# Optimization experiments

Measured on AMD Instinct MI355X. Metric: run time of the kernel, lower is better.

The kernel has to match this reference:

```python
import jax, jax.numpy as jnp
import numpy as np

EPS = 1e-9

def _gumbel_softmax(logits, u):
    # torch: noise.add_(1e-9).log_().neg_() twice -> g = -log(-log(u+eps)+eps)
    g = -jnp.log(-jnp.log(u + EPS) + EPS)
    return jax.nn.softmax(logits + g, axis=-1)  # tau=1, temperature=0

def setup_inputs() -> dict:
    key = jax.random.key(0)
    ks = jax.random.split(key, 8)
    n_obs, n_topics, n_dim, batch = 8192, 128, 64, 8192
    return {
        "pij": jax.random.uniform(ks[0], (batch,), jnp.float32, 1e-6, 1.0),
        "noise_full": jax.random.uniform(ks[1], (n_obs, n_topics), jnp.float32),
        "noise_i": jax.random.uniform(ks[2], (batch, n_topics), jnp.float32),
        "noise_j": jax.random.uniform(ks[3], (batch, n_topics), jnp.float32),
        "logits_weight": jax.random.normal(ks[4], (n_obs, n_topics), jnp.float32),
        "topic_w": jax.random.normal(ks[5], (n_dim, n_topics), jnp.float32) * 0.1,
        "topic_b": jax.random.normal(ks[6], (n_dim,), jnp.float32) * 0.1,
        "i": jax.random.randint(ks[7], (batch,), 0, n_obs),
        "j": jax.random.randint(jax.random.fold_in(key, 7), (batch,), 0, n_obs),
    }

def reference(pij, noise_full, noise_i, noise_j, logits_weight, topic_w, topic_b, i, j):
    topic = lambda z: z @ topic_w.T + topic_b
    # x: [n_obs, n_dim]
    x = topic(_gumbel_softmax(logits_weight, noise_full))
    # pairwise squared distances via norm trick (same math as expand-sub-square-sum)
    sq = jnp.sum(x * x, axis=-1)                      # [n_obs]
    dkl2 = sq[:, None] + sq[None, :] - 2.0 * (x @ x.T)  # [n_obs, n_obs]
    n_diagonal = dkl2.shape[0]
    part = jnp.sum(1.0 / (1.0 + dkl2)) - n_diagonal
    xi = topic(_gumbel_softmax(logits_weight[i], noise_i))  # [B, n_dim]
    xj = topic(_gumbel_softmax(logits_weight[j], noise_j))
    # faithful to source: sum of (1 + diff^2) over dims, then reciprocal
    num = 1.0 / jnp.sum(1.0 + (xi - xj) ** 2, axis=1)
    qij = num / part
    loss_kld = pij * (jnp.log(pij) - jnp.log(qij))
    return loss_kld
```

## Files before the change

### kernel.cpp

```cpp
#include <hip/hip_runtime.h>
#include <hip/hip_bf16.h>


typedef short bf16x8 __attribute__((ext_vector_type(8)));
typedef float f32x4 __attribute__((ext_vector_type(4)));

__device__ __forceinline__ float wave_sum(float v) {
#pragma unroll
  for (int off = 32; off; off >>= 1) v += __shfl_xor(v, off);
  return v;
}

__device__ __forceinline__ unsigned short f2bf(float x) {
  union { float f; unsigned u; } v; v.f = x;
  return (unsigned short)((v.u + 0x7fffu + ((v.u >> 16) & 1u)) >> 16);
}
__device__ __forceinline__ float bf2f(unsigned short h) {
  union { float f; unsigned u; } v; v.u = ((unsigned)h) << 16;
  return v.f;
}

__device__ __forceinline__ void gumbel_mfma(const float* __restrict__ lgp,
                                            const float* __restrict__ nzp,
                                            const bf16x8 Bf[4][4], f32x4 acc[4]) {
  float e[32];
  float ps = 0.0f;
#pragma unroll
  for (int ks = 0; ks < 4; ++ks) {
#pragma unroll
    for (int h = 0; h < 2; ++h) {
      float4 L = *(const float4*)(lgp + ks * 32 + h * 4);
      float4 U = *(const float4*)(nzp + ks * 32 + h * 4);
      float lv[4] = {L.x, L.y, L.z, L.w};
      float uv[4] = {U.x, U.y, U.z, U.w};
#pragma unroll
      for (int j = 0; j < 4; ++j) {
        float g = -__logf(-__logf(uv[j] + 1e-9f) + 1e-9f);
        float ev = __expf(lv[j] + g);
        e[ks * 8 + h * 4 + j] = ev;
        ps += ev;
      }
    }
  }
  ps += __shfl_xor(ps, 16);
  ps += __shfl_xor(ps, 32);
  float inv = __builtin_amdgcn_rcpf(ps);
#pragma unroll
  for (int ks = 0; ks < 4; ++ks) {
    union { bf16x8 v; unsigned short s[8]; } pk;
#pragma unroll
    for (int j = 0; j < 8; ++j) pk.s[j] = f2bf(e[ks * 8 + j] * inv);
#pragma unroll
    for (int nt = 0; nt < 4; ++nt)
      acc[nt] = __builtin_amdgcn_mfma_f32_16x16x32_bf16(pk.v, Bf[nt][ks], acc[nt], 0, 0, 0);
  }
}

__global__ __launch_bounds__(256) void row_engine(
    const float* __restrict__ logits, const float* __restrict__ noise_f,
    const float* __restrict__ noise_i, const float* __restrict__ noise_j,
    const float* __restrict__ topic_w, const float* __restrict__ tb,
    const int* __restrict__ ii, const int* __restrict__ jj,
    unsigned short* __restrict__ xb, float* __restrict__ sq,
    float* __restrict__ denomS) {
  int w = threadIdx.x >> 6, lane = threadIdx.x & 63;
  int r = lane & 15, part = lane >> 4;
  int wid = blockIdx.x * 4 + w;

  bf16x8 Bf[4][4];
#pragma unroll
  for (int nt = 0; nt < 4; ++nt) {
    const float* wp = topic_w + (nt * 16 + r) * 128 + part * 8;
#pragma unroll
    for (int ks = 0; ks < 4; ++ks) {
      float4 w0 = *(const float4*)(wp + ks * 32);
      float4 w1 = *(const float4*)(wp + ks * 32 + 4);
      union { bf16x8 v; unsigned short s[8]; } pk;
      pk.s[0] = f2bf(w0.x); pk.s[1] = f2bf(w0.y); pk.s[2] = f2bf(w0.z); pk.s[3] = f2bf(w0.w);
      pk.s[4] = f2bf(w1.x); pk.s[5] = f2bf(w1.y); pk.s[6] = f2bf(w1.z); pk.s[7] = f2bf(w1.w);
      Bf[nt][ks] = pk.v;
    }
  }
  int grp = wid >> 1;
  if ((wid & 1) == 0) {
    int g16 = grp * 16;
    float tbv[4];
#pragma unroll
    for (int nt = 0; nt < 4; ++nt) tbv[nt] = tb[nt * 16 + r];
    f32x4 acc[4] = {};
    gumbel_mfma(logits + (g16 + r) * 128 + part * 8,
                noise_f + (g16 + r) * 128 + part * 8, Bf, acc);
    float sqp[4] = {0.f, 0.f, 0.f, 0.f};
#pragma unroll
    for (int nt = 0; nt < 4; ++nt)
#pragma unroll
      for (int g = 0; g < 4; ++g) {
        unsigned short hb = f2bf(acc[nt][g] + tbv[nt]);
        xb[(g16 + part * 4 + g) * 64 + nt * 16 + r] = hb;
        float xr = bf2f(hb);
        sqp[g] += xr * xr;
      }
#pragma unroll
    for (int m = 1; m < 16; m <<= 1)
#pragma unroll
      for (int g = 0; g < 4; ++g) sqp[g] += __shfl_xor(sqp[g], m);
    if (r == 0) {
#pragma unroll
      for (int g = 0; g < 4; ++g) sq[g16 + part * 4 + g] = sqp[g];
    }
  } else {
    int b0 = grp * 16;
    int rowi = ii[b0 + r], rowj = jj[b0 + r];
    f32x4 ai[4] = {}, aj[4] = {};
    gumbel_mfma(logits + rowi * 128 + part * 8,
                noise_i + (b0 + r) * 128 + part * 8, Bf, ai);
    gumbel_mfma(logits + rowj * 128 + part * 8,
                noise_j + (b0 + r) * 128 + part * 8, Bf, aj);
    float dp[4] = {0.f, 0.f, 0.f, 0.f};
#pragma unroll
    for (int nt = 0; nt < 4; ++nt)
#pragma unroll
      for (int g = 0; g < 4; ++g) {
        float d = ai[nt][g] - aj[nt][g];
        dp[g] += d * d;
      }
#pragma unroll
    for (int m = 1; m < 16; m <<= 1)
#pragma unroll
      for (int g = 0; g < 4; ++g) dp[g] += __shfl_xor(dp[g], m);
    if (r == 0) {
#pragma unroll
      for (int g = 0; g < 4; ++g) denomS[b0 + part * 4 + g] = 64.0f + dp[g];
    }
  }
}

#define NPAIR_BLOCKS 544
__global__ __launch_bounds__(256) void pairwise(const unsigned short* __restrict__ xbp,
                                                const float* __restrict__ sq,
                                                float* __restrict__ partial) {
  __shared__ float red[4];
  int w = threadIdx.x >> 6, lane = threadIdx.x & 63;
  int b = blockIdx.x, bi = 0, nch = 16;
  while (b >= nch) { b -= nch; ++bi; nch = (64 - bi + 3) >> 2; }
  int cj0 = bi + (b << 2);
  int wr = w >> 1, wc = w & 1;
  int R = bi * 128 + wr * 64;
  int r0 = lane & 15, kq = lane >> 4;

  bf16x8 A[4][2];
#pragma unroll
  for (int a = 0; a < 4; ++a)
#pragma unroll
    for (int s = 0; s < 2; ++s)
      A[a][s] = *(const bf16x8*)(xbp + (R + a * 16 + r0) * 64 + s * 32 + kq * 8);
  float m1[4][4];
#pragma unroll
  for (int a = 0; a < 4; ++a)
#pragma unroll
    for (int g = 0; g < 4; ++g) m1[a][g] = 1.0f + sq[R + a * 16 + kq * 4 + g];

  float local = 0.0f;
  int bjEnd = min(cj0 + 4, 64);
  int bj = cj0;
  if (cj0 == bi && wr > wc) ++bj;
  if (bj < bjEnd) {
    bf16x8 Bc[4][2];
    float nsqc[4];
    {
      int C = bj * 128 + wc * 64;
#pragma unroll
      for (int a = 0; a < 4; ++a)
#pragma unroll
        for (int s = 0; s < 2; ++s)
          Bc[a][s] = *(const bf16x8*)(xbp + (C + a * 16 + r0) * 64 + s * 32 + kq * 8);
#pragma unroll
      for (int q = 0; q < 4; ++q) nsqc[q] = sq[C + q * 16 + r0];
    }
    for (; bj < bjEnd; ++bj) {
      bool hasNext = (bj + 1) < bjEnd;
      bf16x8 Bn[4][2];
      float nsqn[4];
      if (hasNext) {
        int Cn = (bj + 1) * 128 + wc * 64;
#pragma unroll
        for (int a = 0; a < 4; ++a)
#pragma unroll
          for (int s = 0; s < 2; ++s)
            Bn[a][s] = *(const bf16x8*)(xbp + (Cn + a * 16 + r0) * 64 + s * 32 + kq * 8);
#pragma unroll
        for (int q = 0; q < 4; ++q) nsqn[q] = sq[Cn + q * 16 + r0];
      }

      f32x4 acc[4][4] = {};
#pragma unroll
      for (int a = 0; a < 4; ++a)
#pragma unroll
        for (int q = 0; q < 4; ++q) {
          acc[a][q] = __builtin_amdgcn_mfma_f32_16x16x32_bf16(A[a][0], Bc[q][0], acc[a][q], 0, 0, 0);
          acc[a][q] = __builtin_amdgcn_mfma_f32_16x16x32_bf16(A[a][1], Bc[q][1], acc[a][q], 0, 0, 0);
        }

      if (bj == bi && wr == wc) {
#pragma unroll
        for (int a = 0; a < 4; ++a)
#pragma unroll
          for (int q = 0; q < 4; ++q)
#pragma unroll
            for (int g = 0; g < 4; ++g) {
              float d = fmaf(-2.0f, acc[a][q][g], m1[a][g] + nsqc[q]);
              int rl = a * 16 + kq * 4 + g, cl = q * 16 + r0;
              local += (rl < cl) ? __builtin_amdgcn_rcpf(d) : 0.0f;
            }
      } else {
#pragma unroll
        for (int a = 0; a < 4; ++a)
#pragma unroll
          for (int q = 0; q < 4; ++q)
#pragma unroll
            for (int g = 0; g < 4; ++g) {
              float d = fmaf(-2.0f, acc[a][q][g], m1[a][g] + nsqc[q]);
              local += __builtin_amdgcn_rcpf(d);
            }
      }

      if (hasNext) {
#pragma unroll
        for (int a = 0; a < 4; ++a)
#pragma unroll
          for (int s = 0; s < 2; ++s) Bc[a][s] = Bn[a][s];
#pragma unroll
        for (int q = 0; q < 4; ++q) nsqc[q] = nsqn[q];
      }
    }
  }
  local = wave_sum(local);
  if (lane == 0) red[w] = local;
  __syncthreads();
  if (threadIdx.x == 0) partial[blockIdx.x] = red[0] + red[1] + red[2] + red[3];
}

__global__ __launch_bounds__(256) void finalize(const float* __restrict__ pij,
                                                const float* __restrict__ denomS,
                                                const float* __restrict__ partial,
                                                float* __restrict__ out) {
  __shared__ float red[4];
  int tid = threadIdx.x, w = tid >> 6, lane = tid & 63;
  float ps = 0.0f;
  for (int k = tid; k < NPAIR_BLOCKS; k += 256) ps += partial[k];
  ps = wave_sum(ps);
  if (lane == 0) red[w] = ps;
  __syncthreads();
  float part = 2.0f * (red[0] + red[1] + red[2] + red[3]);
  int b = blockIdx.x * 256 + tid;
  float p = pij[b];
  out[b] = p * (__logf(p) + __logf(denomS[b]) + __logf(part));
}

extern "C" void kernel_launch(void* const* d_in, const int* in_sizes, int n_in,
                              void* d_out, int out_size, void* d_ws, size_t ws_size,
                              hipStream_t stream) {
  const float* pij     = (const float*)d_in[0];
  const float* noise_f = (const float*)d_in[1];
  const float* noise_i = (const float*)d_in[2];
  const float* noise_j = (const float*)d_in[3];
  const float* logits  = (const float*)d_in[4];
  const float* topic_w = (const float*)d_in[5];
  const float* tb      = (const float*)d_in[6];
  const int*   ii      = (const int*)d_in[7];
  const int*   jj      = (const int*)d_in[8];
  float* out = (float*)d_out;

  char* ws = (char*)d_ws;
  float* partial     = (float*)ws;
  unsigned short* xb = (unsigned short*)(ws + 8192);
  float* sq          = (float*)(ws + 8192 + 1048576);
  float* denomS      = (float*)(ws + 8192 + 1048576 + 32768);

  row_engine<<<256, 256, 0, stream>>>(logits, noise_f, noise_i, noise_j,
                                      topic_w, tb, ii, jj, xb, sq, denomS);
  pairwise<<<NPAIR_BLOCKS, 256, 0, stream>>>(xb, sq, partial);
  finalize<<<32, 256, 0, stream>>>(pij, denomS, partial, out);
}
```

Before: 112.7 us.

## Fuse row, pairwise and finalize stages into one persistent kernel with grid barriers

Merges the three launches into a single 256-block persistent kernel. Two software grid barriers, built from atomic counters in the workspace, separate the stages. The pairwise tiles are distributed round-robin over the 256 blocks instead of one block per tile. This removes the launch gaps and kernel boundaries between stages, but adds barrier spin-waits and an uneven tile load (2 versus 3 units per block). Counter reset depends on the workspace holding a poison value at launch, so repeated calls without re-poisoning would skip the barriers.

```diff
diff --git a/kernel.cpp b/kernel.cpp
--- a/kernel.cpp
+++ b/kernel.cpp
@@ -4,6 +4,10 @@
 
 typedef short bf16x8 __attribute__((ext_vector_type(8)));
 typedef float f32x4 __attribute__((ext_vector_type(4)));
+
+#define NPAIR_UNITS 544
+#define NBLOCKS 256
+#define POISON32 0xAAAAAAAAu
 
 __device__ __forceinline__ float wave_sum(float v) {
 #pragma unroll
@@ -18,6 +22,19 @@
 __device__ __forceinline__ float bf2f(unsigned short h) {
   union { float f; unsigned u; } v; v.u = ((unsigned)h) << 16;
   return v.f;
+}
+
+__device__ __forceinline__ void grid_barrier(unsigned* cnt) {
+  __syncthreads();
+  if (threadIdx.x == 0) {
+    __threadfence();
+    atomicAdd(cnt, 1u);
+    while (__hip_atomic_load(cnt, __ATOMIC_RELAXED, __HIP_MEMORY_SCOPE_AGENT) <
+           (unsigned)NBLOCKS)
+      __builtin_amdgcn_s_sleep(8);
+    __threadfence();
+  }
+  __syncthreads();
 }
 
 __device__ __forceinline__ void gumbel_mfma(const float* __restrict__ lgp,
@@ -56,205 +73,213 @@
   }
 }
 
-__global__ __launch_bounds__(256) void row_engine(
+__global__ __launch_bounds__(256) void topicsne_fused(
     const float* __restrict__ logits, const float* __restrict__ noise_f,
     const float* __restrict__ noise_i, const float* __restrict__ noise_j,
     const float* __restrict__ topic_w, const float* __restrict__ tb,
     const int* __restrict__ ii, const int* __restrict__ jj,
-    unsigned short* __restrict__ xb, float* __restrict__ sq,
-    float* __restrict__ denomS) {
+    const float* __restrict__ pij, unsigned short* __restrict__ xb,
+    float* __restrict__ sq, float* __restrict__ denomS,
+    float* __restrict__ partial, unsigned* __restrict__ c1,
+    unsigned* __restrict__ c2, float* __restrict__ out) {
+  __shared__ float red[4];
   int w = threadIdx.x >> 6, lane = threadIdx.x & 63;
   int r = lane & 15, part = lane >> 4;
-  int wid = blockIdx.x * 4 + w;
-
-  bf16x8 Bf[4][4];
-#pragma unroll
-  for (int nt = 0; nt < 4; ++nt) {
-    const float* wp = topic_w + (nt * 16 + r) * 128 + part * 8;
-#pragma unroll
-    for (int ks = 0; ks < 4; ++ks) {
-      float4 w0 = *(const float4*)(wp + ks * 32);
-      float4 w1 = *(const float4*)(wp + ks * 32 + 4);
-      union { bf16x8 v; unsigned short s[8]; } pk;
-      pk.s[0] = f2bf(w0.x); pk.s[1] = f2bf(w0.y); pk.s[2] = f2bf(w0.z); pk.s[3] = f2bf(w0.w);
-      pk.s[4] = f2bf(w1.x); pk.s[5] = f2bf(w1.y); pk.s[6] = f2bf(w1.z); pk.s[7] = f2bf(w1.w);
-      Bf[nt][ks] = pk.v;
-    }
-  }
-  int grp = wid >> 1;
-  if ((wid & 1) == 0) {
-    int g16 = grp * 16;
-    float tbv[4];
-#pragma unroll
-    for (int nt = 0; nt < 4; ++nt) tbv[nt] = tb[nt * 16 + r];
-    f32x4 acc[4] = {};
-    gumbel_mfma(logits + (g16 + r) * 128 + part * 8,
-                noise_f + (g16 + r) * 128 + part * 8, Bf, acc);
-    float sqp[4] = {0.f, 0.f, 0.f, 0.f};
-#pragma unroll
-    for (int nt = 0; nt < 4; ++nt)
-#pragma unroll
-      for (int g = 0; g < 4; ++g) {
-        unsigned short hb = f2bf(acc[nt][g] + tbv[nt]);
-        xb[(g16 + part * 4 + g) * 64 + nt * 16 + r] = hb;
-        float xr = bf2f(hb);
-        sqp[g] += xr * xr;
-      }
-#pragma unroll
-    for (int m = 1; m < 16; m <<= 1)
-#pragma unroll
-      for (int g = 0; g < 4; ++g) sqp[g] += __shfl_xor(sqp[g], m);
-    if (r == 0) {
-#pragma unroll
-      for (int g = 0; g < 4; ++g) sq[g16 + part * 4 + g] = sqp[g];
-    }
-  } else {
-    int b0 = grp * 16;
-    int rowi = ii[b0 + r], rowj = jj[b0 + r];
-    f32x4 ai[4] = {}, aj[4] = {};
-    gumbel_mfma(logits + rowi * 128 + part * 8,
-                noise_i + (b0 + r) * 128 + part * 8, Bf, ai);
-    gumbel_mfma(logits + rowj * 128 + part * 8,
-                noise_j + (b0 + r) * 128 + part * 8, Bf, aj);
-    float dp[4] = {0.f, 0.f, 0.f, 0.f};
-#pragma unroll
-    for (int nt = 0; nt < 4; ++nt)
-#pragma unroll
-      for (int g = 0; g < 4; ++g) {
-        float d = ai[nt][g] - aj[nt][g];
-        dp[g] += d * d;
-      }
-#pragma unroll
-    for (int m = 1; m < 16; m <<= 1)
-#pragma unroll
-      for (int g = 0; g < 4; ++g) dp[g] += __shfl_xor(dp[g], m);
-    if (r == 0) {
-#pragma unroll
-      for (int g = 0; g < 4; ++g) denomS[b0 + part * 4 + g] = 64.0f + dp[g];
-    }
-  }
-}
-
-#define NPAIR_BLOCKS 544
-__global__ __launch_bounds__(256) void pairwise(const unsigned short* __restrict__ xbp,
-                                                const float* __restrict__ sq,
-                                                float* __restrict__ partial) {
-  __shared__ float red[4];
-  int w = threadIdx.x >> 6, lane = threadIdx.x & 63;
-  int b = blockIdx.x, bi = 0, nch = 16;
-  while (b >= nch) { b -= nch; ++bi; nch = (64 - bi + 3) >> 2; }
-  int cj0 = bi + (b << 2);
+
+  if (threadIdx.x == 0) {
+    atomicCAS(c1, POISON32, 0u);
+    atomicCAS(c2, POISON32, 0u);
+  }
+
+  {
+    int wid = blockIdx.x * 4 + w;
+    bf16x8 Bf[4][4];
+#pragma unroll
+    for (int nt = 0; nt < 4; ++nt) {
+      const float* wp = topic_w + (nt * 16 + r) * 128 + part * 8;
+#pragma unroll
+      for (int ks = 0; ks < 4; ++ks) {
+        float4 w0 = *(const float4*)(wp + ks * 32);
+        float4 w1 = *(const float4*)(wp + ks * 32 + 4);
+        union { bf16x8 v; unsigned short s[8]; } pk;
+        pk.s[0] = f2bf(w0.x); pk.s[1] = f2bf(w0.y); pk.s[2] = f2bf(w0.z); pk.s[3] = f2bf(w0.w);
+        pk.s[4] = f2bf(w1.x); pk.s[5] = f2bf(w1.y); pk.s[6] = f2bf(w1.z); pk.s[7] = f2bf(w1.w);
+        Bf[nt][ks] = pk.v;
+      }
+    }
+    int grp = wid >> 1;
+    if ((wid & 1) == 0) {
+      int g16 = grp * 16;
+      float tbv[4];
+#pragma unroll
+      for (int nt = 0; nt < 4; ++nt) tbv[nt] = tb[nt * 16 + r];
+      f32x4 acc[4] = {};
+      gumbel_mfma(logits + (g16 + r) * 128 + part * 8,
+                  noise_f + (g16 + r) * 128 + part * 8, Bf, acc);
+      float sqp[4] = {0.f, 0.f, 0.f, 0.f};
+#pragma unroll
+      for (int nt = 0; nt < 4; ++nt)
+#pragma unroll
+        for (int g = 0; g < 4; ++g) {
+          unsigned short hb = f2bf(acc[nt][g] + tbv[nt]);
+          xb[(g16 + part * 4 + g) * 64 + nt * 16 + r] = hb;
+          float xr = bf2f(hb);
+          sqp[g] += xr * xr;
+        }
+#pragma unroll
+      for (int m = 1; m < 16; m <<= 1)
+#pragma unroll
+        for (int g = 0; g < 4; ++g) sqp[g] += __shfl_xor(sqp[g], m);
+      if (r == 0) {
+#pragma unroll
+        for (int g = 0; g < 4; ++g) sq[g16 + part * 4 + g] = sqp[g];
+      }
+    } else {
+      int b0 = grp * 16;
+      int rowi = ii[b0 + r], rowj = jj[b0 + r];
+      f32x4 ai[4] = {}, aj[4] = {};
+      gumbel_mfma(logits + rowi * 128 + part * 8,
+                  noise_i + (b0 + r) * 128 + part * 8, Bf, ai);
+      gumbel_mfma(logits + rowj * 128 + part * 8,
+                  noise_j + (b0 + r) * 128 + part * 8, Bf, aj);
+      float dp[4] = {0.f, 0.f, 0.f, 0.f};
+#pragma unroll
+      for (int nt = 0; nt < 4; ++nt)
+#pragma unroll
+        for (int g = 0; g < 4; ++g) {
+          float d = ai[nt][g] - aj[nt][g];
+          dp[g] += d * d;
+        }
+#pragma unroll
+      for (int m = 1; m < 16; m <<= 1)
+#pragma unroll
+        for (int g = 0; g < 4; ++g) dp[g] += __shfl_xor(dp[g], m);
+      if (r == 0) {
+#pragma unroll
+        for (int g = 0; g < 4; ++g) denomS[b0 + part * 4 + g] = 64.0f + dp[g];
+      }
+    }
+  }
+
+  grid_barrier(c1);
+
   int wr = w >> 1, wc = w & 1;
-  int R = bi * 128 + wr * 64;
   int r0 = lane & 15, kq = lane >> 4;
-
-  bf16x8 A[4][2];
-#pragma unroll
-  for (int a = 0; a < 4; ++a)
-#pragma unroll
-    for (int s = 0; s < 2; ++s)
-      A[a][s] = *(const bf16x8*)(xbp + (R + a * 16 + r0) * 64 + s * 32 + kq * 8);
-  float m1[4][4];
-#pragma unroll
-  for (int a = 0; a < 4; ++a)
-#pragma unroll
-    for (int g = 0; g < 4; ++g) m1[a][g] = 1.0f + sq[R + a * 16 + kq * 4 + g];
-
-  float local = 0.0f;
-  int bjEnd = min(cj0 + 4, 64);
-  int bj = cj0;
-  if (cj0 == bi && wr > wc) ++bj;
-  if (bj < bjEnd) {
-    bf16x8 Bc[4][2];
-    float nsqc[4];
-    {
-      int C = bj * 128 + wc * 64;
-#pragma unroll
-      for (int a = 0; a < 4; ++a)
-#pragma unroll
-        for (int s = 0; s < 2; ++s)
-          Bc[a][s] = *(const bf16x8*)(xbp + (C + a * 16 + r0) * 64 + s * 32 + kq * 8);
-#pragma unroll
-      for (int q = 0; q < 4; ++q) nsqc[q] = sq[C + q * 16 + r0];
-    }
-    for (; bj < bjEnd; ++bj) {
-      bool hasNext = (bj + 1) < bjEnd;
-      bf16x8 Bn[4][2];
-      float nsqn[4];
-      if (hasNext) {
-        int Cn = (bj + 1) * 128 + wc * 64;
+  for (int u = blockIdx.x; u < NPAIR_UNITS; u += NBLOCKS) {
+    int b = u, bi = 0, nch = 16;
+    while (b >= nch) { b -= nch; ++bi; nch = (64 - bi + 3) >> 2; }
+    int cj0 = bi + (b << 2);
+    int R = bi * 128 + wr * 64;
+
+    bf16x8 A[4][2];
+#pragma unroll
+    for (int a = 0; a < 4; ++a)
+#pragma unroll
+      for (int s = 0; s < 2; ++s)
+        A[a][s] = *(const bf16x8*)(xb + (R + a * 16 + r0) * 64 + s * 32 + kq * 8);
+    float m1[4][4];
+#pragma unroll
+    for (int a = 0; a < 4; ++a)
+#pragma unroll
+      for (int g = 0; g < 4; ++g) m1[a][g] = 1.0f + sq[R + a * 16 + kq * 4 + g];
+
+    float local = 0.0f;
+    int bjEnd = min(cj0 + 4, 64);
+    int bj = cj0;
+    if (cj0 == bi && wr > wc) ++bj;
+    if (bj < bjEnd) {
+      bf16x8 Bc[4][2];
+      float nsqc[4];
+      {
+        int C = bj * 128 + wc * 64;
 #pragma unroll
         for (int a = 0; a < 4; ++a)
 #pragma unroll
           for (int s = 0; s < 2; ++s)
-            Bn[a][s] = *(const bf16x8*)(xbp + (Cn + a * 16 + r0) * 64 + s * 32 + kq * 8);
-#pragma unroll
-        for (int q = 0; q < 4; ++q) nsqn[q] = sq[Cn + q * 16 + r0];
-      }
-
-      f32x4 acc[4][4] = {};
-#pragma unroll
-      for (int a = 0; a < 4; ++a)
-#pragma unroll
-        for (int q = 0; q < 4; ++q) {
-          acc[a][q] = __builtin_amdgcn_mfma_f32_16x16x32_bf16(A[a][0], Bc[q][0], acc[a][q], 0, 0, 0);
-          acc[a][q] = __builtin_amdgcn_mfma_f32_16x16x32_bf16(A[a][1], Bc[q][1], acc[a][q], 0, 0, 0);
-        }
-
-      if (bj == bi && wr == wc) {
+            Bc[a][s] = *(const bf16x8*)(xb + (C + a * 16 + r0) * 64 + s * 32 + kq * 8);
+#pragma unroll
+        for (int q = 0; q < 4; ++q) nsqc[q] = sq[C + q * 16 + r0];
+      }
+      for (; bj < bjEnd; ++bj) {
+        bool hasNext = (bj + 1) < bjEnd;
+        bf16x8 Bn[4][2];
+        float nsqn[4];
+        if (hasNext) {
+          int Cn = (bj + 1) * 128 + wc * 64;
+#pragma unroll
+          for (int a = 0; a < 4; ++a)
+#pragma unroll
+            for (int s = 0; s < 2; ++s)
+              Bn[a][s] = *(const bf16x8*)(xb + (Cn + a * 16 + r0) * 64 + s * 32 + kq * 8);
+#pragma unroll
+          for (int q = 0; q < 4; ++q) nsqn[q] = sq[Cn + q * 16 + r0];
+        }
+
+        f32x4 acc[4][4] = {};
 #pragma unroll
         for (int a = 0; a < 4; ++a)
 #pragma unroll
-          for (int q = 0; q < 4; ++q)
-#pragma unroll
-            for (int g = 0; g < 4; ++g) {
-              float d = fmaf(-2.0f, acc[a][q][g], m1[a][g] + nsqc[q]);
-              int rl = a * 16 + kq * 4 + g, cl = q * 16 + r0;
-              local += (rl < cl) ? __builtin_amdgcn_rcpf(d) : 0.0f;
-            }
-      } else {
-#pragma unroll
-        for (int a = 0; a < 4; ++a)
-#pragma unroll
-          for (int q = 0; q < 4; ++q)
-#pragma unroll
-            for (int g = 0; g < 4; ++g) {
-              float d = fmaf(-2.0f, acc[a][q][g], m1[a][g] + nsqc[q]);
-              local += __builtin_amdgcn_rcpf(d);
-            }
-      }
-
-      if (hasNext) {
-#pragma unroll
-        for (int a = 0; a < 4; ++a)
-#pragma unroll
-          for (int s = 0; s < 2; ++s) Bc[a][s] = Bn[a][s];
-#pragma unroll
-        for (int q = 0; q < 4; ++q) nsqc[q] = nsqn[q];
-      }
-    }
-  }
-  local = wave_sum(local);
-  if (lane == 0) red[w] = local;
-  __syncthreads();
-  if (threadIdx.x == 0) partial[blockIdx.x] = red[0] + red[1] + red[2] + red[3];
-}
-
-__global__ __launch_bounds__(256) void finalize(const float* __restrict__ pij,
-                                                const float* __restrict__ denomS,
-                                                const float* __restrict__ partial,
-                                                float* __restrict__ out) {
-  __shared__ float red[4];
-  int tid = threadIdx.x, w = tid >> 6, lane = tid & 63;
-  float ps = 0.0f;
-  for (int k = tid; k < NPAIR_BLOCKS; k += 256) ps += partial[k];
-  ps = wave_sum(ps);
-  if (lane == 0) red[w] = ps;
-  __syncthreads();
-  float part = 2.0f * (red[0] + red[1] + red[2] + red[3]);
-  int b = blockIdx.x * 256 + tid;
-  float p = pij[b];
-  out[b] = p * (__logf(p) + __logf(denomS[b]) + __logf(part));
+          for (int q = 0; q < 4; ++q) {
+            acc[a][q] = __builtin_amdgcn_mfma_f32_16x16x32_bf16(A[a][0], Bc[q][0], acc[a][q], 0, 0, 0);
+            acc[a][q] = __builtin_amdgcn_mfma_f32_16x16x32_bf16(A[a][1], Bc[q][1], acc[a][q], 0, 0, 0);
+          }
+
+        if (bj == bi && wr == wc) {
+#pragma unroll
+          for (int a = 0; a < 4; ++a)
+#pragma unroll
+            for (int q = 0; q < 4; ++q)
+#pragma unroll
+              for (int g = 0; g < 4; ++g) {
+                float d = fmaf(-2.0f, acc[a][q][g], m1[a][g] + nsqc[q]);
+                int rl = a * 16 + kq * 4 + g, cl = q * 16 + r0;
+                local += (rl < cl) ? __builtin_amdgcn_rcpf(d) : 0.0f;
+              }
+        } else {
+#pragma unroll
+          for (int a = 0; a < 4; ++a)
+#pragma unroll
+            for (int q = 0; q < 4; ++q)
+#pragma unroll
+              for (int g = 0; g < 4; ++g) {
+                float d = fmaf(-2.0f, acc[a][q][g], m1[a][g] + nsqc[q]);
+                local += __builtin_amdgcn_rcpf(d);
+              }
+        }
+
+        if (hasNext) {
+#pragma unroll
+          for (int a = 0; a < 4; ++a)
+#pragma unroll
+            for (int s = 0; s < 2; ++s) Bc[a][s] = Bn[a][s];
+#pragma unroll
+          for (int q = 0; q < 4; ++q) nsqc[q] = nsqn[q];
+        }
+      }
+    }
+    local = wave_sum(local);
+    if (lane == 0) red[w] = local;
+    __syncthreads();
+    if (threadIdx.x == 0) partial[u] = red[0] + red[1] + red[2] + red[3];
+    __syncthreads();
+  }
+
+  grid_barrier(c2);
+
+  {
+    float ps = 0.0f;
+    for (int k = threadIdx.x; k < NPAIR_UNITS; k += 256) ps += partial[k];
+    ps = wave_sum(ps);
+    if (lane == 0) red[w] = ps;
+    __syncthreads();
+    float partv = 2.0f * (red[0] + red[1] + red[2] + red[3]);
+    float lp = __logf(partv);
+    int b = blockIdx.x * 32 + (threadIdx.x & 31);
+    if ((threadIdx.x >> 5) == 0) {
+      float p = pij[b];
+      out[b] = p * (__logf(p) + __logf(denomS[b]) + lp);
+    }
+  }
 }
 
 extern "C" void kernel_launch(void* const* d_in, const int* in_sizes, int n_in,
@@ -273,12 +298,13 @@
 
   char* ws = (char*)d_ws;
   float* partial     = (float*)ws;
+  unsigned* c1       = (unsigned*)(ws + 4096);
+  unsigned* c2       = (unsigned*)(ws + 4096 + 128);
   unsigned short* xb = (unsigned short*)(ws + 8192);
   float* sq          = (float*)(ws + 8192 + 1048576);
   float* denomS      = (float*)(ws + 8192 + 1048576 + 32768);
 
-  row_engine<<<256, 256, 0, stream>>>(logits, noise_f, noise_i, noise_j,
-                                      topic_w, tb, ii, jj, xb, sq, denomS);
-  pairwise<<<NPAIR_BLOCKS, 256, 0, stream>>>(xb, sq, partial);
-  finalize<<<32, 256, 0, stream>>>(pij, denomS, partial, out);
-}
+  topicsne_fused<<<NBLOCKS, 256, 0, stream>>>(
+      logits, noise_f, noise_i, noise_j, topic_w, tb, ii, jj, pij,
+      xb, sq, denomS, partial, c1, c2, out);
+}
```

After: 146.8 us. 1.3x slower.

## Stage row_engine inputs into LDS via async global_load_lds before compute

Applied to the files above, without the earlier changes.

Each block now copies topic_w, the logits rows (including gathered i/j rows) and the noise rows into shared memory with global_load_lds, coalesced 16-byte per lane, then synchronises once and computes the Gumbel softmax and MFMA from LDS. This targets the strided, partly uncoalesced per-lane float4 global loads and the repeated per-wave topic_w reads. In exchange it uses 128 KB of LDS per block, which limits occupancy to about one block per CU, and adds a block-wide barrier.

```diff
diff --git a/kernel.cpp b/kernel.cpp
--- a/kernel.cpp
+++ b/kernel.cpp
@@ -20,26 +20,30 @@
   return v.f;
 }
 
-__device__ __forceinline__ void gumbel_mfma(const float* __restrict__ lgp,
-                                            const float* __restrict__ nzp,
-                                            const bf16x8 Bf[4][4], f32x4 acc[4]) {
+__device__ __forceinline__ void ld_lds16(const float* g, float* l) {
+  __builtin_amdgcn_global_load_lds(
+      (const __attribute__((address_space(1))) void*)g,
+      (__attribute__((address_space(3))) void*)l, 16, 0, 0);
+}
+
+__device__ __forceinline__ void gs_compute_lds(const float* Lb, const float* Ub,
+                                               const bf16x8 Bf[4][4],
+                                               int r, int part, f32x4 acc[4]) {
   float e[32];
   float ps = 0.0f;
 #pragma unroll
-  for (int ks = 0; ks < 4; ++ks) {
-#pragma unroll
-    for (int h = 0; h < 2; ++h) {
-      float4 L = *(const float4*)(lgp + ks * 32 + h * 4);
-      float4 U = *(const float4*)(nzp + ks * 32 + h * 4);
-      float lv[4] = {L.x, L.y, L.z, L.w};
-      float uv[4] = {U.x, U.y, U.z, U.w};
-#pragma unroll
-      for (int j = 0; j < 4; ++j) {
-        float g = -__logf(-__logf(uv[j] + 1e-9f) + 1e-9f);
-        float ev = __expf(lv[j] + g);
-        e[ks * 8 + h * 4 + j] = ev;
-        ps += ev;
-      }
+  for (int q = 0; q < 8; ++q) {
+    int off = r * 128 + (q >> 1) * 32 + part * 8 + (q & 1) * 4;
+    float4 L = *(const float4*)(Lb + off);
+    float4 U = *(const float4*)(Ub + off);
+    float lv[4] = {L.x, L.y, L.z, L.w};
+    float uv[4] = {U.x, U.y, U.z, U.w};
+#pragma unroll
+    for (int j = 0; j < 4; ++j) {
+      float g = -__logf(-__logf(uv[j] + 1e-9f) + 1e-9f);
+      float ev = __expf(lv[j] + g);
+      e[q * 4 + j] = ev;
+      ps += ev;
     }
   }
   ps += __shfl_xor(ps, 16);
@@ -63,14 +67,54 @@
     const int* __restrict__ ii, const int* __restrict__ jj,
     unsigned short* __restrict__ xb, float* __restrict__ sq,
     float* __restrict__ denomS) {
+  __shared__ __align__(16) float sh[32768];
   int w = threadIdx.x >> 6, lane = threadIdx.x & 63;
   int r = lane & 15, part = lane >> 4;
   int wid = blockIdx.x * 4 + w;
+  int grp = wid >> 1;
+  int lsub = lane & 31;
+  int rhalf = lane >> 5;
+
+#pragma unroll
+  for (int t2 = 0; t2 < 8; ++t2) {
+    int t = w * 8 + t2;
+    ld_lds16(topic_w + (2 * t + rhalf) * 128 + lsub * 4, &sh[t * 256]);
+  }
+
+  float* reg = &sh[8192 + (w >> 1) * 12288 + (w & 1) * 4096];
+
+  if ((w & 1) == 0) {
+    int g16 = grp * 16;
+#pragma unroll
+    for (int t = 0; t < 8; ++t) {
+      int row = g16 + 2 * t + rhalf;
+      ld_lds16(logits + row * 128 + lsub * 4, reg + t * 256);
+      ld_lds16(noise_f + row * 128 + lsub * 4, reg + 2048 + t * 256);
+    }
+  } else {
+    int b0 = grp * 16;
+    int rowiv = ii[b0 + r], rowjv = jj[b0 + r];
+#pragma unroll
+    for (int t = 0; t < 8; ++t) {
+      int brow = b0 + 2 * t + rhalf;
+      ld_lds16(noise_i + brow * 128 + lsub * 4, reg + 2048 + t * 256);
+      ld_lds16(noise_j + brow * 128 + lsub * 4, reg + 6144 + t * 256);
+    }
+#pragma unroll
+    for (int t = 0; t < 8; ++t) {
+      int ri = __shfl(rowiv, 2 * t + rhalf);
+      int rj = __shfl(rowjv, 2 * t + rhalf);
+      ld_lds16(logits + ri * 128 + lsub * 4, reg + t * 256);
+      ld_lds16(logits + rj * 128 + lsub * 4, reg + 4096 + t * 256);
+    }
+  }
+
+  __syncthreads();
 
   bf16x8 Bf[4][4];
 #pragma unroll
   for (int nt = 0; nt < 4; ++nt) {
-    const float* wp = topic_w + (nt * 16 + r) * 128 + part * 8;
+    const float* wp = &sh[(nt * 16 + r) * 128 + part * 8];
 #pragma unroll
     for (int ks = 0; ks < 4; ++ks) {
       float4 w0 = *(const float4*)(wp + ks * 32);
@@ -81,15 +125,14 @@
       Bf[nt][ks] = pk.v;
     }
   }
-  int grp = wid >> 1;
-  if ((wid & 1) == 0) {
+
+  if ((w & 1) == 0) {
     int g16 = grp * 16;
     float tbv[4];
 #pragma unroll
     for (int nt = 0; nt < 4; ++nt) tbv[nt] = tb[nt * 16 + r];
     f32x4 acc[4] = {};
-    gumbel_mfma(logits + (g16 + r) * 128 + part * 8,
-                noise_f + (g16 + r) * 128 + part * 8, Bf, acc);
+    gs_compute_lds(reg, reg + 2048, Bf, r, part, acc);
     float sqp[4] = {0.f, 0.f, 0.f, 0.f};
 #pragma unroll
     for (int nt = 0; nt < 4; ++nt)
@@ -110,12 +153,9 @@
     }
   } else {
     int b0 = grp * 16;
-    int rowi = ii[b0 + r], rowj = jj[b0 + r];
     f32x4 ai[4] = {}, aj[4] = {};
-    gumbel_mfma(logits + rowi * 128 + part * 8,
-                noise_i + (b0 + r) * 128 + part * 8, Bf, ai);
-    gumbel_mfma(logits + rowj * 128 + part * 8,
-                noise_j + (b0 + r) * 128 + part * 8, Bf, aj);
+    gs_compute_lds(reg, reg + 2048, Bf, r, part, ai);
+    gs_compute_lds(reg + 4096, reg + 6144, Bf, r, part, aj);
     float dp[4] = {0.f, 0.f, 0.f, 0.f};
 #pragma unroll
     for (int nt = 0; nt < 4; ++nt)
```

New measurement: 113.9 us. Within noise of the previous version (+1.1%).
